# Optimization experiments

Measured on AMD Instinct MI355X. Metric: run time of the kernel, lower is better.

## Reference

```python
import jax, jax.numpy as jnp
from jax import lax
import numpy as np

B, T, D, H, C = 256, 2048, 40, 128, 35
LN_EPS = 1e-5


def _uniform(key, shape, scale):
    return jax.random.uniform(key, shape, jnp.float32, -scale, scale)


def setup_inputs() -> dict:
    key = jax.random.key(0)
    ks = jax.random.split(key, 16)
    s = 1.0 / np.sqrt(H)  # PyTorch LSTM init scale
    inp = {
        "x": jax.random.normal(ks[0], (B, T, D), jnp.float32),
        "length": jax.random.randint(ks[1], (B,), 1, T + 1, jnp.int32),
        # layer 0 (input_size=D)
        "W_ih0": _uniform(ks[2], (4 * H, D), s),
        "W_hh0": _uniform(ks[3], (4 * H, H), s),
        "b_ih0": _uniform(ks[4], (4 * H,), s),
        "b_hh0": _uniform(ks[5], (4 * H,), s),
        # layer 1 (input_size=H)
        "W_ih1": _uniform(ks[6], (4 * H, H), s),
        "W_hh1": _uniform(ks[7], (4 * H, H), s),
        "b_ih1": _uniform(ks[8], (4 * H,), s),
        "b_hh1": _uniform(ks[9], (4 * H,), s),
        # LayerNorm + Linear head
        "ln_gamma": jnp.ones((H,), jnp.float32),
        "ln_beta": jnp.zeros((H,), jnp.float32),
        "fc_w": _uniform(ks[10], (C, H), 1.0 / np.sqrt(H)),
        "fc_b": _uniform(ks[11], (C,), 1.0 / np.sqrt(H)),
    }
    return inp


def _lstm_layer(xs, length, W_ih, W_hh, b_ih, b_hh):
    # xs: [T, B, D_in]; masked recurrence emulates pack_padded_sequence:
    # state is frozen for t >= length, so the final h equals the state at
    # each sequence's last valid step.
    Tn, Bn = xs.shape[0], xs.shape[1]
    Hn = W_hh.shape[1]
    h0 = jnp.zeros((Bn, Hn), xs.dtype)
    c0 = jnp.zeros((Bn, Hn), xs.dtype)

    def step(carry, inp):
        h, c = carry
        x_t, t = inp
        gates = x_t @ W_ih.T + b_ih + h @ W_hh.T + b_hh  # [B, 4H]
        i, f, g, o = jnp.split(gates, 4, axis=-1)  # PyTorch gate order i,f,g,o
        i = jax.nn.sigmoid(i)
        f = jax.nn.sigmoid(f)
        g = jnp.tanh(g)
        o = jax.nn.sigmoid(o)
        c_new = f * c + i * g
        h_new = o * jnp.tanh(c_new)
        m = (t < length)[:, None]
        h = jnp.where(m, h_new, h)
        c = jnp.where(m, c_new, c)
        return (h, c), h

    (h_fin, c_fin), hs = lax.scan(step, (h0, c0), (xs, jnp.arange(Tn)))
    return hs, h_fin


def reference(x, length, W_ih0, W_hh0, b_ih0, b_hh0, W_ih1, W_hh1, b_ih1, b_hh1,
              ln_gamma, ln_beta, fc_w, fc_b):
    xs = jnp.transpose(x, (1, 0, 2))  # [T, B, D]
    hs1, _ = _lstm_layer(xs, length, W_ih0, W_hh0, b_ih0, b_hh0)
    _, h_last = _lstm_layer(hs1, length, W_ih1, W_hh1, b_ih1, b_hh1)  # h[-1]: [B, H]
    # LayerNorm over feature dim
    mu = jnp.mean(h_last, axis=-1, keepdims=True)
    var = jnp.mean(jnp.square(h_last - mu), axis=-1, keepdims=True)
    hn = (h_last - mu) * lax.rsqrt(var + LN_EPS) * ln_gamma + ln_beta
    return hn @ fc_w.T + fc_b  # [B, C]
```

## Files before the change

### kernel.cpp

```cpp
#include <hip/hip_runtime.h>

#define Bn 256
#define Tn 2048
#define Dn 40
#define Hn 128
#define Cn 35

typedef _Float16 h2 __attribute__((ext_vector_type(2)));

__device__ __forceinline__ int sdot4(int a, int b, int c) {
#if __has_builtin(__builtin_amdgcn_sdot4)
  return __builtin_amdgcn_sdot4(a, b, c, false);
#else
  int r = c;
#pragma unroll
  for (int i = 0; i < 4; ++i)
    r += ((int)(a << (24 - 8 * i)) >> 24) * ((int)(b << (24 - 8 * i)) >> 24);
  return r;
#endif
}

__device__ __forceinline__ float fdot2f(h2 a, h2 b, float c) {
#if __has_builtin(__builtin_amdgcn_fdot2)
  return __builtin_amdgcn_fdot2(a, b, c, false);
#else
  return c + (float)(a[0]) * (float)(b[0]) + (float)(a[1]) * (float)(b[1]);
#endif
}

__device__ __forceinline__ h2 bch(int u) { return __builtin_bit_cast(h2, u); }

__device__ __forceinline__ int pk2i(float a, float b) {
  h2 r; r[0] = (_Float16)a; r[1] = (_Float16)b;
  return __builtin_bit_cast(int, r);
}

__device__ __forceinline__ float rcpf_(float x) {
#if __has_builtin(__builtin_amdgcn_rcpf)
  return __builtin_amdgcn_rcpf(x);
#else
  return 1.f / x;
#endif
}

__device__ __forceinline__ float sigm(float v) {
  v = fmaxf(fminf(v, 60.f), -60.f);
  return rcpf_(1.f + __expf(-v));
}

__device__ __forceinline__ float tanha(float v) {
  v = fmaxf(fminf(v, 15.f), -15.f);
  const float e = __expf(2.f * v);
  return (e - 1.f) * rcpf_(e + 1.f);
}

__device__ __forceinline__ int q8c(float v) {
  v = fminf(fmaxf(v, -127.f), 127.f);
  return (int)__builtin_rintf(v);
}

__device__ __forceinline__ int pk4(int a, int b, int c, int d) {
  return (a & 255) | ((b & 255) << 8) | ((c & 255) << 16) | (d << 24);
}

#if __has_builtin(__builtin_amdgcn_global_load_lds)
#define HAVE_GLDS 1
__device__ __forceinline__ void gl_lds16(const float* g, float* l) {
  __builtin_amdgcn_global_load_lds(
      (const __attribute__((address_space(1))) unsigned int*)(const void*)g,
      (__attribute__((address_space(3))) unsigned int*)(void*)l, 16, 0, 0);
}
#endif

__device__ __forceinline__ void quantW128(const float* __restrict__ p,
                                          int* __restrict__ q, float& sc) {
  float m = 1e-30f;
#pragma unroll
  for (int i = 0; i < 32; ++i) {
    const float4 v = reinterpret_cast<const float4*>(p)[i];
    m = fmaxf(m, fmaxf(fmaxf(fabsf(v.x), fabsf(v.y)),
                       fmaxf(fabsf(v.z), fabsf(v.w))));
  }
  const float inv = 127.f / m;
  sc = m * (1.f / 127.f);
#pragma unroll
  for (int i = 0; i < 32; ++i) {
    const float4 v = reinterpret_cast<const float4*>(p)[i];
    q[i] = pk4(q8c(v.x * inv), q8c(v.y * inv), q8c(v.z * inv), q8c(v.w * inv));
  }
}

#define RLST(w) __builtin_amdgcn_readlane(                                  \
    ((w) < 64 ? st0 : (w) < 128 ? st1 : (w) < 192 ? st2 : (w) < 256 ? st3  \
                                                        : st4), (w) & 63)

__global__ __launch_bounds__(512) void lstm2_fused(
    const float* __restrict__ x,
    const int*   __restrict__ length,
    const float* __restrict__ Wih0, const float* __restrict__ Whh0,
    const float* __restrict__ bih0, const float* __restrict__ bhh0,
    const float* __restrict__ Wih1, const float* __restrict__ Whh1,
    const float* __restrict__ bih1, const float* __restrict__ bhh1,
    const float* __restrict__ gam,  const float* __restrict__ bet,
    const float* __restrict__ fcw,  const float* __restrict__ fcb,
    float* __restrict__ out)
{
  __shared__ int   s_w0x[20][512];
  __shared__ __align__(16) float s_xraw[192 * 4];
  __shared__ int   s_xh2[2][320];
  __shared__ float s_xp[2][16][512];
  __shared__ float s_p0[4][132];
  __shared__ float s_p1[4][132];
  __shared__ int   s_hq[64];
  __shared__ float s_h1f[128];
  __shared__ float s_hn[128];

  const int tid  = threadIdx.x;
  const int lane = tid & 63;
  const int b    = blockIdx.x;
  const int len  = length[b];

  if (tid >= 256 && tid < 448) {
    const int seg0 = (tid >> 6) - 4;
    int seg = seg0 * 64 + lane;
    if (seg >= 160) seg = 0;
#if HAVE_GLDS
    gl_lds16(x + (size_t)b * Tn * Dn + seg * 4, &s_xraw[seg0 * 256]);
#else
    *(float4*)&s_xraw[seg * 4] =
        *(const float4*)(x + (size_t)b * Tn * Dn + seg * 4);
#endif
  }

  int q0h[32], q1x[32], q1h[32];
  float s0h, s1x, s1h;
  quantW128(Whh0 + (size_t)tid * Hn, q0h, s0h);
  quantW128(Wih1 + (size_t)tid * Hn, q1x, s1x);
  quantW128(Whh1 + (size_t)tid * Hn, q1h, s1h);
  s0h *= (1.f / 127.f);
  s1x *= (1.f / 127.f);
  s1h *= (1.f / 127.f);
  {
    const float* p = Wih0 + (size_t)tid * Dn;
#pragma unroll
    for (int k = 0; k < 20; ++k) s_w0x[k][tid] = pk2i(p[2 * k], p[2 * k + 1]);
  }
  const float bias0 = bih0[tid] + bhh0[tid];
  const float bias1 = bih1[tid] + bhh1[tid];

  float c0 = 0.f;
  float c1 = 0.f;

  if (tid < 64) s_hq[tid] = 0;
  __syncthreads();

  auto burst = [&](int bb) {
    const int* flat = &s_xh2[bb][0];
    const int st0 = flat[lane], st1 = flat[lane + 64], st2 = flat[lane + 128],
              st3 = flat[lane + 192], st4 = flat[lane + 256];
#pragma unroll
    for (int pass = 0; pass < 4; ++pass) {
      float a0 = 0.f, a1 = 0.f, a2 = 0.f, a3 = 0.f;
      const int r0 = pass * 4;
#pragma unroll
      for (int g = 0; g < 5; ++g) {
        const h2 w0 = bch(s_w0x[4 * g + 0][tid]);
        const h2 w1 = bch(s_w0x[4 * g + 1][tid]);
        const h2 w2 = bch(s_w0x[4 * g + 2][tid]);
        const h2 w3 = bch(s_w0x[4 * g + 3][tid]);
        a0 = fdot2f(bch(RLST(20 * (r0 + 0) + 4 * g + 0)), w0, a0);
        a0 = fdot2f(bch(RLST(20 * (r0 + 0) + 4 * g + 1)), w1, a0);
        a0 = fdot2f(bch(RLST(20 * (r0 + 0) + 4 * g + 2)), w2, a0);
        a0 = fdot2f(bch(RLST(20 * (r0 + 0) + 4 * g + 3)), w3, a0);
        a1 = fdot2f(bch(RLST(20 * (r0 + 1) + 4 * g + 0)), w0, a1);
        a1 = fdot2f(bch(RLST(20 * (r0 + 1) + 4 * g + 1)), w1, a1);
        a1 = fdot2f(bch(RLST(20 * (r0 + 1) + 4 * g + 2)), w2, a1);
        a1 = fdot2f(bch(RLST(20 * (r0 + 1) + 4 * g + 3)), w3, a1);
        a2 = fdot2f(bch(RLST(20 * (r0 + 2) + 4 * g + 0)), w0, a2);
        a2 = fdot2f(bch(RLST(20 * (r0 + 2) + 4 * g + 1)), w1, a2);
        a2 = fdot2f(bch(RLST(20 * (r0 + 2) + 4 * g + 2)), w2, a2);
        a2 = fdot2f(bch(RLST(20 * (r0 + 2) + 4 * g + 3)), w3, a2);
        a3 = fdot2f(bch(RLST(20 * (r0 + 3) + 4 * g + 0)), w0, a3);
        a3 = fdot2f(bch(RLST(20 * (r0 + 3) + 4 * g + 1)), w1, a3);
        a3 = fdot2f(bch(RLST(20 * (r0 + 3) + 4 * g + 2)), w2, a3);
        a3 = fdot2f(bch(RLST(20 * (r0 + 3) + 4 * g + 3)), w3, a3);
      }
      s_xp[bb][r0 + 0][tid] = a0;
      s_xp[bb][r0 + 1][tid] = a1;
      s_xp[bb][r0 + 2][tid] = a2;
      s_xp[bb][r0 + 3][tid] = a3;
    }
  };

  if (tid >= 256 && tid < 416) {
    const int u = tid - 256;
    const float4 v = *(const float4*)&s_xraw[4 * u];
    s_xh2[0][2 * u]     = pk2i(v.x, v.y);
    s_xh2[0][2 * u + 1] = pk2i(v.z, v.w);
  }
  __syncthreads();
  burst(0);
  __syncthreads();
  s_p0[tid >> 7][tid & 127] = bias0 + s_xp[0][0][tid];
  __syncthreads();

#pragma unroll 1
  for (int t = 0; t < len; ++t) {
    const int tl = t & 15;

    if (tid < 128) {
      const float gi = s_p0[0][tid], gf = s_p0[1][tid];
      const float gg = s_p0[2][tid], go = s_p0[3][tid];
      c0 = sigm(gf) * c0 + sigm(gi) * tanha(gg);
      const float h = sigm(go) * tanha(c0);
      ((signed char*)s_hq)[tid] = (signed char)(int)__builtin_rintf(h * 127.f);
    } else if (tid < 256) {
      if (t > 0) {
        const int u = tid - 128;
        const float gi = s_p1[0][u], gf = s_p1[1][u];
        const float gg = s_p1[2][u], go = s_p1[3][u];
        c1 = sigm(gf) * c1 + sigm(gi) * tanha(gg);
        const float h = sigm(go) * tanha(c1);
        ((signed char*)s_hq)[128 + u] =
            (signed char)(int)__builtin_rintf(h * 127.f);
      }
    } else if (tid < 416 && tl == 13) {
      const int u = tid - 256;
      const float4 v = *(const float4*)&s_xraw[4 * u];
      const int nb = ((t + 3) >> 4) & 1;
      s_xh2[nb][2 * u]     = pk2i(v.x, v.y);
      s_xh2[nb][2 * u + 1] = pk2i(v.z, v.w);
    }
    __syncthreads();

    const int vq = s_hq[lane];

    if (tid >= 256 && tid < 448 && tl == 12) {
      const int t0 = (t & ~15) + 16;
      if (t0 <= Tn - 16) {
        const int seg0 = (tid >> 6) - 4;
        int seg = seg0 * 64 + lane;
        if (seg >= 160) seg = 0;
#if HAVE_GLDS
        gl_lds16(x + ((size_t)b * Tn + t0) * Dn + seg * 4,
                 &s_xraw[seg0 * 256]);
#else
        *(float4*)&s_xraw[seg * 4] =
            *(const float4*)(x + ((size_t)b * Tn + t0) * Dn + seg * 4);
#endif
      }
    }

    const int rowi = t + 1;
    const float xacc = s_xp[(rowi >> 4) & 1][rowi & 15][tid];

    int ia = 0, ia2 = 0, ib = 0, ib2 = 0, ic = 0, ic2 = 0;
#pragma unroll
    for (int j = 0; j < 32; j += 2) {
      const int s0 = __builtin_amdgcn_readlane(vq, j);
      const int s1 = __builtin_amdgcn_readlane(vq, j + 1);
      ia  = sdot4(s0, q0h[j], ia);
      ib  = sdot4(s0, q1x[j], ib);
      ia2 = sdot4(s1, q0h[j + 1], ia2);
      ib2 = sdot4(s1, q1x[j + 1], ib2);
    }
#pragma unroll
    for (int j = 0; j < 32; j += 2) {
      const int s0 = __builtin_amdgcn_readlane(vq, 32 + j);
      const int s1 = __builtin_amdgcn_readlane(vq, 33 + j);
      ic  = sdot4(s0, q1h[j], ic);
      ic2 = sdot4(s1, q1h[j + 1], ic2);
    }
    s_p0[tid >> 7][tid & 127] = bias0 + xacc + (float)(ia + ia2) * s0h;
    s_p1[tid >> 7][tid & 127] =
        bias1 + (float)(ib + ib2) * s1x + (float)(ic + ic2) * s1h;

    if (tl == 14) burst(((t + 2) >> 4) & 1);
    __syncthreads();
  }

  if (tid >= 128 && tid < 256) {
    const int u = tid - 128;
    const float gi = s_p1[0][u], gf = s_p1[1][u];
    const float gg = s_p1[2][u], go = s_p1[3][u];
    c1 = sigm(gf) * c1 + sigm(gi) * tanha(gg);
    s_h1f[u] = sigm(go) * tanha(c1);
  }
  __syncthreads();

  if (tid < 64) {
    const float a = s_h1f[tid], d = s_h1f[64 + tid];
    float s = a + d, q = a * a + d * d;
#pragma unroll
    for (int m = 32; m >= 1; m >>= 1) {
      s += __shfl_xor(s, m, 64);
      q += __shfl_xor(q, m, 64);
    }
    const float mu = s * (1.f / 128.f);
    float var = q * (1.f / 128.f) - mu * mu;
    var = fmaxf(var, 0.f);
    const float rstd = rsqrtf(var + 1e-5f);
    s_hn[tid]      = (a - mu) * rstd * gam[tid]      + bet[tid];
    s_hn[64 + tid] = (d - mu) * rstd * gam[64 + tid] + bet[64 + tid];
  }
  __syncthreads();

  if (tid < Cn) {
    float acc = fcb[tid];
    const float* wp = fcw + tid * Hn;
#pragma unroll 4
    for (int k = 0; k < Hn; ++k) acc += s_hn[k] * wp[k];
    out[(size_t)b * Cn + tid] = acc;
  }
}

extern "C" void kernel_launch(void* const* d_in, const int* in_sizes, int n_in,
                              void* d_out, int out_size, void* d_ws, size_t ws_size,
                              hipStream_t stream) {
  (void)in_sizes; (void)n_in; (void)d_ws; (void)ws_size; (void)out_size;
  lstm2_fused<<<dim3(Bn), dim3(512), 0, stream>>>(
      (const float*)d_in[0],  (const int*)d_in[1],
      (const float*)d_in[2],  (const float*)d_in[3],
      (const float*)d_in[4],  (const float*)d_in[5],
      (const float*)d_in[6],  (const float*)d_in[7],
      (const float*)d_in[8],  (const float*)d_in[9],
      (const float*)d_in[10], (const float*)d_in[11],
      (const float*)d_in[12], (const float*)d_in[13],
      (float*)d_out);
}
```

Baseline: 2.512 ms.

## Split LSTM layers across waves with shuffle gate exchange and one barrier per step

Reassigns the work so waves 0-3 own layer 0 and waves 4-7 own layer 1. Each lane computes two gate rows and exchanges gates with its partner lane through a cross-lane shuffle, instead of writing gate pre-activations to shared memory and re-reading them after a barrier. The hidden-state buffer is double-buffered, which cuts the barriers per timestep from two to one; the raw barrier is issued with an explicit waitcnt. The cost is imbalance: layer-1 waves now do twice the dot-product work of layer-0 waves, and register pressure rises with four quantized weight arrays per lane.

```diff
diff --git a/kernel.cpp b/kernel.cpp
--- a/kernel.cpp
+++ b/kernel.cpp
@@ -109,19 +109,23 @@
   __shared__ __align__(16) float s_xraw[192 * 4];
   __shared__ int   s_xh2[2][320];
   __shared__ float s_xp[2][16][512];
-  __shared__ float s_p0[4][132];
-  __shared__ float s_p1[4][132];
-  __shared__ int   s_hq[64];
+  __shared__ int   s_hq[2][64];
   __shared__ float s_h1f[128];
   __shared__ float s_hn[128];
 
   const int tid  = threadIdx.x;
   const int lane = tid & 63;
+  const int wv   = tid >> 6;
   const int b    = blockIdx.x;
   const int len  = length[b];
 
-  if (tid >= 256 && tid < 448) {
-    const int seg0 = (tid >> 6) - 4;
+  const bool isL1 = (wv >= 4);
+  const int  u    = ((wv & 3) << 5) | (lane & 31);
+  const int  rA   = ((lane < 32) ? 0 : 256) + u;
+  const int  rB   = rA + 128;
+
+  if (tid < 192) {
+    const int seg0 = wv;
     int seg = seg0 * 64 + lane;
     if (seg >= 160) seg = 0;
 #if HAVE_GLDS
@@ -132,26 +136,33 @@
 #endif
   }
 
-  int q0h[32], q1x[32], q1h[32];
-  float s0h, s1x, s1h;
-  quantW128(Whh0 + (size_t)tid * Hn, q0h, s0h);
-  quantW128(Wih1 + (size_t)tid * Hn, q1x, s1x);
-  quantW128(Whh1 + (size_t)tid * Hn, q1h, s1h);
-  s0h *= (1.f / 127.f);
-  s1x *= (1.f / 127.f);
-  s1h *= (1.f / 127.f);
+  int qA[32], qB[32], qC[32], qD[32];
+  float scA, scB, scC = 0.f, scD = 0.f;
+  float biasA, biasB;
+  if (!isL1) {
+    quantW128(Whh0 + (size_t)rA * Hn, qA, scA);
+    quantW128(Whh0 + (size_t)rB * Hn, qB, scB);
+    biasA = bih0[rA] + bhh0[rA];
+    biasB = bih0[rB] + bhh0[rB];
+  } else {
+    quantW128(Wih1 + (size_t)rA * Hn, qA, scA);
+    quantW128(Wih1 + (size_t)rB * Hn, qB, scB);
+    quantW128(Whh1 + (size_t)rA * Hn, qC, scC);
+    quantW128(Whh1 + (size_t)rB * Hn, qD, scD);
+    biasA = bih1[rA] + bhh1[rA];
+    biasB = bih1[rB] + bhh1[rB];
+  }
+  scA *= (1.f / 127.f);
+  scB *= (1.f / 127.f);
+  scC *= (1.f / 127.f);
+  scD *= (1.f / 127.f);
   {
     const float* p = Wih0 + (size_t)tid * Dn;
 #pragma unroll
     for (int k = 0; k < 20; ++k) s_w0x[k][tid] = pk2i(p[2 * k], p[2 * k + 1]);
   }
-  const float bias0 = bih0[tid] + bhh0[tid];
-  const float bias1 = bih1[tid] + bhh1[tid];
-
-  float c0 = 0.f;
-  float c1 = 0.f;
-
-  if (tid < 64) s_hq[tid] = 0;
+  if (tid < 128) s_hq[tid >> 6][tid & 63] = 0;
+  float creg = 0.f;
   __syncthreads();
 
   auto burst = [&](int bb) {
@@ -192,53 +203,24 @@
     }
   };
 
-  if (tid >= 256 && tid < 416) {
-    const int u = tid - 256;
-    const float4 v = *(const float4*)&s_xraw[4 * u];
-    s_xh2[0][2 * u]     = pk2i(v.x, v.y);
-    s_xh2[0][2 * u + 1] = pk2i(v.z, v.w);
+  if (tid < 160) {
+    const float4 v = *(const float4*)&s_xraw[4 * tid];
+    s_xh2[0][2 * tid]     = pk2i(v.x, v.y);
+    s_xh2[0][2 * tid + 1] = pk2i(v.z, v.w);
   }
   __syncthreads();
   burst(0);
-  __syncthreads();
-  s_p0[tid >> 7][tid & 127] = bias0 + s_xp[0][0][tid];
   __syncthreads();
 
 #pragma unroll 1
   for (int t = 0; t < len; ++t) {
     const int tl = t & 15;
-
-    if (tid < 128) {
-      const float gi = s_p0[0][tid], gf = s_p0[1][tid];
-      const float gg = s_p0[2][tid], go = s_p0[3][tid];
-      c0 = sigm(gf) * c0 + sigm(gi) * tanha(gg);
-      const float h = sigm(go) * tanha(c0);
-      ((signed char*)s_hq)[tid] = (signed char)(int)__builtin_rintf(h * 127.f);
-    } else if (tid < 256) {
-      if (t > 0) {
-        const int u = tid - 128;
-        const float gi = s_p1[0][u], gf = s_p1[1][u];
-        const float gg = s_p1[2][u], go = s_p1[3][u];
-        c1 = sigm(gf) * c1 + sigm(gi) * tanha(gg);
-        const float h = sigm(go) * tanha(c1);
-        ((signed char*)s_hq)[128 + u] =
-            (signed char)(int)__builtin_rintf(h * 127.f);
-      }
-    } else if (tid < 416 && tl == 13) {
-      const int u = tid - 256;
-      const float4 v = *(const float4*)&s_xraw[4 * u];
-      const int nb = ((t + 3) >> 4) & 1;
-      s_xh2[nb][2 * u]     = pk2i(v.x, v.y);
-      s_xh2[nb][2 * u + 1] = pk2i(v.z, v.w);
-    }
-    __syncthreads();
-
-    const int vq = s_hq[lane];
-
-    if (tid >= 256 && tid < 448 && tl == 12) {
+    const int vq = s_hq[t & 1][lane];
+
+    if (tl == 12 && tid < 192) {
       const int t0 = (t & ~15) + 16;
       if (t0 <= Tn - 16) {
-        const int seg0 = (tid >> 6) - 4;
+        const int seg0 = wv;
         int seg = seg0 * 64 + lane;
         if (seg >= 160) seg = 0;
 #if HAVE_GLDS
@@ -250,41 +232,112 @@
 #endif
       }
     }
-
-    const int rowi = t + 1;
-    const float xacc = s_xp[(rowi >> 4) & 1][rowi & 15][tid];
-
-    int ia = 0, ia2 = 0, ib = 0, ib2 = 0, ic = 0, ic2 = 0;
+    if (tl == 13 && tid < 160) {
+#if HAVE_GLDS
+      asm volatile("s_waitcnt vmcnt(0)" ::: "memory");
+#endif
+      const float4 v = *(const float4*)&s_xraw[4 * tid];
+      const int nb = ((t + 3) >> 4) & 1;
+      s_xh2[nb][2 * tid]     = pk2i(v.x, v.y);
+      s_xh2[nb][2 * tid + 1] = pk2i(v.z, v.w);
+    }
+
+    float gv1, gv2;
+    if (!isL1) {
+      int ia = 0, ia2 = 0, ib = 0, ib2 = 0;
+#pragma unroll
+      for (int j = 0; j < 32; j += 2) {
+        const int s0 = __builtin_amdgcn_readlane(vq, j);
+        const int s1 = __builtin_amdgcn_readlane(vq, j + 1);
+        ia  = sdot4(s0, qA[j],     ia);
+        ib  = sdot4(s0, qB[j],     ib);
+        ia2 = sdot4(s1, qA[j + 1], ia2);
+        ib2 = sdot4(s1, qB[j + 1], ib2);
+      }
+      const float xa = s_xp[(t >> 4) & 1][tl][rA];
+      const float xb = s_xp[(t >> 4) & 1][tl][rB];
+      gv1 = biasA + xa + (float)(ia + ia2) * scA;
+      gv2 = biasB + xb + (float)(ib + ib2) * scB;
+    } else {
+      int ia = 0, ia2 = 0, ib = 0, ib2 = 0, ic = 0, ic2 = 0, id_ = 0, id2 = 0;
+#pragma unroll
+      for (int j = 0; j < 32; j += 2) {
+        const int s0 = __builtin_amdgcn_readlane(vq, j);
+        const int s1 = __builtin_amdgcn_readlane(vq, j + 1);
+        ia  = sdot4(s0, qA[j],     ia);
+        ib  = sdot4(s0, qB[j],     ib);
+        ia2 = sdot4(s1, qA[j + 1], ia2);
+        ib2 = sdot4(s1, qB[j + 1], ib2);
+      }
+#pragma unroll
+      for (int j = 0; j < 32; j += 2) {
+        const int s0 = __builtin_amdgcn_readlane(vq, 32 + j);
+        const int s1 = __builtin_amdgcn_readlane(vq, 33 + j);
+        ic  = sdot4(s0, qC[j],     ic);
+        id_ = sdot4(s0, qD[j],     id_);
+        ic2 = sdot4(s1, qC[j + 1], ic2);
+        id2 = sdot4(s1, qD[j + 1], id2);
+      }
+      gv1 = biasA + (float)(ia + ia2) * scA + (float)(ic + ic2) * scC;
+      gv2 = biasB + (float)(ib + ib2) * scB + (float)(id_ + id2) * scD;
+    }
+
+    const float p1 = __shfl_xor(gv1, 32, 64);
+    const float p2 = __shfl_xor(gv2, 32, 64);
+    const bool  lo = (lane < 32);
+    const float gi = lo ? gv1 : p1;
+    const float gf = lo ? gv2 : p2;
+    const float gg = lo ? p1 : gv1;
+    const float go = lo ? p2 : gv2;
+
+    if (!isL1 || t > 0) {
+      creg = sigm(gf) * creg + sigm(gi) * tanha(gg);
+      const float h = sigm(go) * tanha(creg);
+      if (lo)
+        ((signed char*)s_hq)[(((t + 1) & 1) << 8) + (isL1 ? 128 : 0) + u] =
+            (signed char)(int)__builtin_rintf(h * 127.f);
+    }
+
+    if (tl == 14) burst(((t + 2) >> 4) & 1);
+
+    asm volatile("s_waitcnt lgkmcnt(0)" ::: "memory");
+    __builtin_amdgcn_s_barrier();
+    __builtin_amdgcn_sched_barrier(0);
+  }
+
+  if (isL1) {
+    const int vq = s_hq[len & 1][lane];
+    int ia = 0, ia2 = 0, ib = 0, ib2 = 0, ic = 0, ic2 = 0, id_ = 0, id2 = 0;
 #pragma unroll
     for (int j = 0; j < 32; j += 2) {
       const int s0 = __builtin_amdgcn_readlane(vq, j);
       const int s1 = __builtin_amdgcn_readlane(vq, j + 1);
-      ia  = sdot4(s0, q0h[j], ia);
-      ib  = sdot4(s0, q1x[j], ib);
-      ia2 = sdot4(s1, q0h[j + 1], ia2);
-      ib2 = sdot4(s1, q1x[j + 1], ib2);
+      ia  = sdot4(s0, qA[j],     ia);
+      ib  = sdot4(s0, qB[j],     ib);
+      ia2 = sdot4(s1, qA[j + 1], ia2);
+      ib2 = sdot4(s1, qB[j + 1], ib2);
     }
 #pragma unroll
     for (int j = 0; j < 32; j += 2) {
       const int s0 = __builtin_amdgcn_readlane(vq, 32 + j);
       const int s1 = __builtin_amdgcn_readlane(vq, 33 + j);
-      ic  = sdot4(s0, q1h[j], ic);
-      ic2 = sdot4(s1, q1h[j + 1], ic2);
-    }
-    s_p0[tid >> 7][tid & 127] = bias0 + xacc + (float)(ia + ia2) * s0h;
-    s_p1[tid >> 7][tid & 127] =
-        bias1 + (float)(ib + ib2) * s1x + (float)(ic + ic2) * s1h;
-
-    if (tl == 14) burst(((t + 2) >> 4) & 1);
-    __syncthreads();
-  }
-
-  if (tid >= 128 && tid < 256) {
-    const int u = tid - 128;
-    const float gi = s_p1[0][u], gf = s_p1[1][u];
-    const float gg = s_p1[2][u], go = s_p1[3][u];
-    c1 = sigm(gf) * c1 + sigm(gi) * tanha(gg);
-    s_h1f[u] = sigm(go) * tanha(c1);
+      ic  = sdot4(s0, qC[j],     ic);
+      id_ = sdot4(s0, qD[j],     id_);
+      ic2 = sdot4(s1, qC[j + 1], ic2);
+      id2 = sdot4(s1, qD[j + 1], id2);
+    }
+    float gv1 = biasA + (float)(ia + ia2) * scA + (float)(ic + ic2) * scC;
+    float gv2 = biasB + (float)(ib + ib2) * scB + (float)(id_ + id2) * scD;
+    const float p1 = __shfl_xor(gv1, 32, 64);
+    const float p2 = __shfl_xor(gv2, 32, 64);
+    const bool  lo = (lane < 32);
+    const float gi = lo ? gv1 : p1;
+    const float gf = lo ? gv2 : p2;
+    const float gg = lo ? p1 : gv1;
+    const float go = lo ? p2 : gv2;
+    creg = sigm(gf) * creg + sigm(gi) * tanha(gg);
+    const float h = sigm(go) * tanha(creg);
+    if (lo) s_h1f[u] = h;
   }
   __syncthreads();
 
```

New measurement: 2.614 ms. 4.1% more time.

## Replace block barriers with per-wave flag-based pipeline across LSTM layers

Applied to the files above, without the earlier changes.

Each wave now has a fixed role. Waves 0-1 run the layer-0 recurrence over all four gates, waves 2-3 run the layer-1 recurrence, and waves 4-7 compute the layer-1 input projection from h0 and the x-projection bursts. The per-step __syncthreads is replaced by LDS progress flags that each wave polls with spin-waits, so layer 1 can trail layer 0 by up to four steps through a ring buffer of terms. This removes full-block barriers and the extra shared-memory round trip for gates, at the cost of busy-wait polling, more registers per thread, and subtle ordering risks in the hand-written LDS flag protocol.

```diff
diff --git a/kernel.cpp b/kernel.cpp
--- a/kernel.cpp
+++ b/kernel.cpp
@@ -7,6 +7,9 @@
 #define Cn 35
 
 typedef _Float16 h2 __attribute__((ext_vector_type(2)));
+typedef int int4v __attribute__((ext_vector_type(4)));
+
+__device__ __forceinline__ int imin(int a, int b) { return a < b ? a : b; }
 
 __device__ __forceinline__ int sdot4(int a, int b, int c) {
 #if __has_builtin(__builtin_amdgcn_sdot4)
@@ -105,23 +108,24 @@
     const float* __restrict__ fcw,  const float* __restrict__ fcb,
     float* __restrict__ out)
 {
-  __shared__ int   s_w0x[20][512];
   __shared__ __align__(16) float s_xraw[192 * 4];
   __shared__ int   s_xh2[2][320];
   __shared__ float s_xp[2][16][512];
-  __shared__ float s_p0[4][132];
-  __shared__ float s_p1[4][132];
-  __shared__ int   s_hq[64];
+  __shared__ float s_term[4][128][4];
+  __shared__ int   s_h0q[2][32];
+  __shared__ int   s_h1q[2][32];
+  __shared__ __align__(32) int s_flag[8];
   __shared__ float s_h1f[128];
   __shared__ float s_hn[128];
 
   const int tid  = threadIdx.x;
   const int lane = tid & 63;
+  const int wv   = tid >> 6;
   const int b    = blockIdx.x;
   const int len  = length[b];
 
-  if (tid >= 256 && tid < 448) {
-    const int seg0 = (tid >> 6) - 4;
+  if (wv >= 4 && wv <= 6) {
+    const int seg0 = wv - 4;
     int seg = seg0 * 64 + lane;
     if (seg >= 160) seg = 0;
 #if HAVE_GLDS
@@ -131,161 +135,260 @@
         *(const float4*)(x + (size_t)b * Tn * Dn + seg * 4);
 #endif
   }
-
-  int q0h[32], q1x[32], q1h[32];
-  float s0h, s1x, s1h;
-  quantW128(Whh0 + (size_t)tid * Hn, q0h, s0h);
-  quantW128(Wih1 + (size_t)tid * Hn, q1x, s1x);
-  quantW128(Whh1 + (size_t)tid * Hn, q1h, s1h);
-  s0h *= (1.f / 127.f);
-  s1x *= (1.f / 127.f);
-  s1h *= (1.f / 127.f);
-  {
-    const float* p = Wih0 + (size_t)tid * Dn;
-#pragma unroll
-    for (int k = 0; k < 20; ++k) s_w0x[k][tid] = pk2i(p[2 * k], p[2 * k + 1]);
-  }
-  const float bias0 = bih0[tid] + bhh0[tid];
-  const float bias1 = bih1[tid] + bhh1[tid];
-
-  float c0 = 0.f;
-  float c1 = 0.f;
-
-  if (tid < 64) s_hq[tid] = 0;
+  if (tid < 32) {
+    s_h0q[0][tid] = 0; s_h0q[1][tid] = 0;
+    s_h1q[0][tid] = 0; s_h1q[1][tid] = 0;
+  }
+  if (tid < 8) s_flag[tid] = 0;
+
+  int qq0[32], qq1[32], qq2[32], qq3[32];
+  int wpa[20], wpb[20];
+  float sc0 = 0.f, sc1 = 0.f, sc2 = 0.f, sc3 = 0.f;
+  float bs0 = 0.f, bs1 = 0.f, bs2 = 0.f, bs3 = 0.f;
+
+  if (wv < 2) {
+    const int u = (wv << 6) | lane;
+    quantW128(Whh0 + (size_t)(u)       * Hn, qq0, sc0);
+    quantW128(Whh0 + (size_t)(u + 128) * Hn, qq1, sc1);
+    quantW128(Whh0 + (size_t)(u + 256) * Hn, qq2, sc2);
+    quantW128(Whh0 + (size_t)(u + 384) * Hn, qq3, sc3);
+    bs0 = bih0[u]       + bhh0[u];
+    bs1 = bih0[u + 128] + bhh0[u + 128];
+    bs2 = bih0[u + 256] + bhh0[u + 256];
+    bs3 = bih0[u + 384] + bhh0[u + 384];
+  } else if (wv < 4) {
+    const int u = ((wv - 2) << 6) | lane;
+    quantW128(Whh1 + (size_t)(u)       * Hn, qq0, sc0);
+    quantW128(Whh1 + (size_t)(u + 128) * Hn, qq1, sc1);
+    quantW128(Whh1 + (size_t)(u + 256) * Hn, qq2, sc2);
+    quantW128(Whh1 + (size_t)(u + 384) * Hn, qq3, sc3);
+  } else {
+    const int hl = ((wv - 4) << 6) | lane;
+    quantW128(Wih1 + (size_t)hl * Hn, qq0, sc0);
+    quantW128(Wih1 + (size_t)(hl + 256) * Hn, qq1, sc1);
+    bs0 = bih1[hl]       + bhh1[hl];
+    bs1 = bih1[hl + 256] + bhh1[hl + 256];
+    const float* p0 = Wih0 + (size_t)hl * Dn;
+    const float* p1 = Wih0 + (size_t)(hl + 256) * Dn;
+#pragma unroll
+    for (int k = 0; k < 20; ++k) {
+      wpa[k] = pk2i(p0[2 * k], p0[2 * k + 1]);
+      wpb[k] = pk2i(p1[2 * k], p1[2 * k + 1]);
+    }
+  }
+  sc0 *= (1.f / 127.f);
+  sc1 *= (1.f / 127.f);
+  sc2 *= (1.f / 127.f);
+  sc3 *= (1.f / 127.f);
+
   __syncthreads();
 
-  auto burst = [&](int bb) {
-    const int* flat = &s_xh2[bb][0];
+  if (wv >= 4) {
+    const int hl = ((wv - 4) << 6) | lane;
+    if (hl < 160) {
+      const float4 v = *(const float4*)&s_xraw[4 * hl];
+      s_xh2[0][2 * hl]     = pk2i(v.x, v.y);
+      s_xh2[0][2 * hl + 1] = pk2i(v.z, v.w);
+    }
+  }
+  __syncthreads();
+
+  if (wv >= 4) {
+    const int hl = ((wv - 4) << 6) | lane;
+    const int* flat = &s_xh2[0][0];
     const int st0 = flat[lane], st1 = flat[lane + 64], st2 = flat[lane + 128],
               st3 = flat[lane + 192], st4 = flat[lane + 256];
-#pragma unroll
-    for (int pass = 0; pass < 4; ++pass) {
-      float a0 = 0.f, a1 = 0.f, a2 = 0.f, a3 = 0.f;
-      const int r0 = pass * 4;
-#pragma unroll
-      for (int g = 0; g < 5; ++g) {
-        const h2 w0 = bch(s_w0x[4 * g + 0][tid]);
-        const h2 w1 = bch(s_w0x[4 * g + 1][tid]);
-        const h2 w2 = bch(s_w0x[4 * g + 2][tid]);
-        const h2 w3 = bch(s_w0x[4 * g + 3][tid]);
-        a0 = fdot2f(bch(RLST(20 * (r0 + 0) + 4 * g + 0)), w0, a0);
-        a0 = fdot2f(bch(RLST(20 * (r0 + 0) + 4 * g + 1)), w1, a0);
-        a0 = fdot2f(bch(RLST(20 * (r0 + 0) + 4 * g + 2)), w2, a0);
-        a0 = fdot2f(bch(RLST(20 * (r0 + 0) + 4 * g + 3)), w3, a0);
-        a1 = fdot2f(bch(RLST(20 * (r0 + 1) + 4 * g + 0)), w0, a1);
-        a1 = fdot2f(bch(RLST(20 * (r0 + 1) + 4 * g + 1)), w1, a1);
-        a1 = fdot2f(bch(RLST(20 * (r0 + 1) + 4 * g + 2)), w2, a1);
-        a1 = fdot2f(bch(RLST(20 * (r0 + 1) + 4 * g + 3)), w3, a1);
-        a2 = fdot2f(bch(RLST(20 * (r0 + 2) + 4 * g + 0)), w0, a2);
-        a2 = fdot2f(bch(RLST(20 * (r0 + 2) + 4 * g + 1)), w1, a2);
-        a2 = fdot2f(bch(RLST(20 * (r0 + 2) + 4 * g + 2)), w2, a2);
-        a2 = fdot2f(bch(RLST(20 * (r0 + 2) + 4 * g + 3)), w3, a2);
-        a3 = fdot2f(bch(RLST(20 * (r0 + 3) + 4 * g + 0)), w0, a3);
-        a3 = fdot2f(bch(RLST(20 * (r0 + 3) + 4 * g + 1)), w1, a3);
-        a3 = fdot2f(bch(RLST(20 * (r0 + 3) + 4 * g + 2)), w2, a3);
-        a3 = fdot2f(bch(RLST(20 * (r0 + 3) + 4 * g + 3)), w3, a3);
-      }
-      s_xp[bb][r0 + 0][tid] = a0;
-      s_xp[bb][r0 + 1][tid] = a1;
-      s_xp[bb][r0 + 2][tid] = a2;
-      s_xp[bb][r0 + 3][tid] = a3;
-    }
-  };
-
-  if (tid >= 256 && tid < 416) {
-    const int u = tid - 256;
-    const float4 v = *(const float4*)&s_xraw[4 * u];
-    s_xh2[0][2 * u]     = pk2i(v.x, v.y);
-    s_xh2[0][2 * u + 1] = pk2i(v.z, v.w);
+#pragma unroll 1
+    for (int r = 0; r < 16; ++r) {
+      float a0 = 0.f, a1 = 0.f;
+#pragma unroll
+      for (int w = 0; w < 20; ++w) {
+        const h2 s = bch(RLST(20 * r + w));
+        a0 = fdot2f(s, bch(wpa[w]), a0);
+        a1 = fdot2f(s, bch(wpb[w]), a1);
+      }
+      s_xp[0][r][hl]       = a0;
+      s_xp[0][r][hl + 256] = a1;
+    }
   }
   __syncthreads();
-  burst(0);
-  __syncthreads();
-  s_p0[tid >> 7][tid & 127] = bias0 + s_xp[0][0][tid];
-  __syncthreads();
-
+
+  const __attribute__((address_space(3))) int* flagp3 =
+      (const __attribute__((address_space(3))) int*)(const void*)s_flag;
+  int4v f03 = {0, 0, 0, 0}, f47 = {0, 0, 0, 0};
+
+#define READFLAGS()                                                          \
+  asm volatile("ds_read_b128 %0, %2\n\tds_read_b128 %1, %2 offset:16\n\t"    \
+               "s_waitcnt lgkmcnt(0)"                                        \
+               : "=v"(f03), "=v"(f47) : "v"(flagp3) : "memory")
+#define HMIN4 imin(imin(f47[0], f47[1]), imin(f47[2], f47[3]))
+#define PUBLISH(val)                                                         \
+  do {                                                                       \
+    asm volatile("s_waitcnt lgkmcnt(0)" ::: "memory");                       \
+    ((volatile int*)s_flag)[wv] = (val);                                     \
+  } while (0)
+
+  if (wv < 2) {
+    const int u = (wv << 6) | lane;
+    float c0 = 0.f;
 #pragma unroll 1
-  for (int t = 0; t < len; ++t) {
-    const int tl = t & 15;
-
-    if (tid < 128) {
-      const float gi = s_p0[0][tid], gf = s_p0[1][tid];
-      const float gg = s_p0[2][tid], go = s_p0[3][tid];
+    for (int t = 0; t < len; ++t) {
+      const int tl = t & 15;
+      const int needH = t - (tl == 0 ? 0 : 1);
+      {
+        int pf = (wv == 0) ? f03[1] : f03[0];
+        if (!(pf >= t && HMIN4 >= needH)) {
+          for (;;) {
+            READFLAGS();
+            pf = (wv == 0) ? f03[1] : f03[0];
+            if (pf >= t && HMIN4 >= needH) break;
+            __builtin_amdgcn_s_sleep(1);
+          }
+        }
+      }
+      const int vq = s_h0q[(t + 1) & 1][lane & 31];
+      const int cs = (t >> 4) & 1;
+      const float xI = s_xp[cs][tl][u];
+      const float xF = s_xp[cs][tl][u + 128];
+      const float xG = s_xp[cs][tl][u + 256];
+      const float xO = s_xp[cs][tl][u + 384];
+      int aI = 0, aF = 0, aG = 0, aO = 0;
+#pragma unroll
+      for (int j = 0; j < 32; ++j) {
+        const int s = __builtin_amdgcn_readlane(vq, j);
+        aI = sdot4(s, qq0[j], aI);
+        aF = sdot4(s, qq1[j], aF);
+        aG = sdot4(s, qq2[j], aG);
+        aO = sdot4(s, qq3[j], aO);
+      }
+      const float gi = bs0 + xI + (float)aI * sc0;
+      const float gf = bs1 + xF + (float)aF * sc1;
+      const float gg = bs2 + xG + (float)aG * sc2;
+      const float go = bs3 + xO + (float)aO * sc3;
       c0 = sigm(gf) * c0 + sigm(gi) * tanha(gg);
       const float h = sigm(go) * tanha(c0);
-      ((signed char*)s_hq)[tid] = (signed char)(int)__builtin_rintf(h * 127.f);
-    } else if (tid < 256) {
-      if (t > 0) {
-        const int u = tid - 128;
-        const float gi = s_p1[0][u], gf = s_p1[1][u];
-        const float gg = s_p1[2][u], go = s_p1[3][u];
-        c1 = sigm(gf) * c1 + sigm(gi) * tanha(gg);
-        const float h = sigm(go) * tanha(c1);
-        ((signed char*)s_hq)[128 + u] =
-            (signed char)(int)__builtin_rintf(h * 127.f);
-      }
-    } else if (tid < 416 && tl == 13) {
-      const int u = tid - 256;
-      const float4 v = *(const float4*)&s_xraw[4 * u];
-      const int nb = ((t + 3) >> 4) & 1;
-      s_xh2[nb][2 * u]     = pk2i(v.x, v.y);
-      s_xh2[nb][2 * u + 1] = pk2i(v.z, v.w);
-    }
-    __syncthreads();
-
-    const int vq = s_hq[lane];
-
-    if (tid >= 256 && tid < 448 && tl == 12) {
-      const int t0 = (t & ~15) + 16;
-      if (t0 <= Tn - 16) {
-        const int seg0 = (tid >> 6) - 4;
-        int seg = seg0 * 64 + lane;
-        if (seg >= 160) seg = 0;
+      ((signed char*)s_h0q)[((t & 1) << 7) + u] =
+          (signed char)(int)__builtin_rintf(h * 127.f);
+      PUBLISH(t + 1);
+      READFLAGS();
+    }
+  } else if (wv < 4) {
+    const int u = ((wv - 2) << 6) | lane;
+    float c1 = 0.f;
+#pragma unroll 1
+    for (int t = 0; t < len; ++t) {
+      {
+        int pf = (wv == 2) ? f03[3] : f03[2];
+        if (!(pf >= t && HMIN4 >= t + 1)) {
+          for (;;) {
+            READFLAGS();
+            pf = (wv == 2) ? f03[3] : f03[2];
+            if (pf >= t && HMIN4 >= t + 1) break;
+            __builtin_amdgcn_s_sleep(1);
+          }
+        }
+      }
+      const int vq = s_h1q[(t + 1) & 1][lane & 31];
+      const float4 tv = *(const float4*)&s_term[t & 3][u][0];
+      int aI = 0, aF = 0, aG = 0, aO = 0;
+#pragma unroll
+      for (int j = 0; j < 32; ++j) {
+        const int s = __builtin_amdgcn_readlane(vq, j);
+        aI = sdot4(s, qq0[j], aI);
+        aF = sdot4(s, qq1[j], aF);
+        aG = sdot4(s, qq2[j], aG);
+        aO = sdot4(s, qq3[j], aO);
+      }
+      const float gi = tv.x + (float)aI * sc0;
+      const float gf = tv.y + (float)aF * sc1;
+      const float gg = tv.z + (float)aG * sc2;
+      const float go = tv.w + (float)aO * sc3;
+      c1 = sigm(gf) * c1 + sigm(gi) * tanha(gg);
+      const float h = sigm(go) * tanha(c1);
+      if (t == len - 1) s_h1f[u] = h;
+      ((signed char*)s_h1q)[((t & 1) << 7) + u] =
+          (signed char)(int)__builtin_rintf(h * 127.f);
+      PUBLISH(t + 1);
+      READFLAGS();
+    }
+  } else {
+    const int hl   = ((wv - 4) << 6) | lane;
+    const int u    = hl & 127;
+    const int gsel = hl >> 7;
+#pragma unroll 1
+    for (int t = 0; t < len; ++t) {
+      const int tl = t & 15;
+      const int needX = (tl == 5) ? (t - 5) : (tl == 8) ? t : -1000000000;
+      if (!(f03[0] >= t + 1 && f03[1] >= t + 1 &&
+            f03[2] >= t - 3 && f03[3] >= t - 3 && HMIN4 >= needX)) {
+        for (;;) {
+          READFLAGS();
+          if (f03[0] >= t + 1 && f03[1] >= t + 1 &&
+              f03[2] >= t - 3 && f03[3] >= t - 3 && HMIN4 >= needX) break;
+          __builtin_amdgcn_s_sleep(1);
+        }
+      }
+      if (tl == 2 && wv <= 6) {
+        const int t0 = (t & ~15) + 16;
+        if (t0 <= Tn - 16) {
+          const int seg0 = wv - 4;
+          int seg = seg0 * 64 + lane;
+          if (seg >= 160) seg = 0;
 #if HAVE_GLDS
-        gl_lds16(x + ((size_t)b * Tn + t0) * Dn + seg * 4,
-                 &s_xraw[seg0 * 256]);
+          gl_lds16(x + ((size_t)b * Tn + t0) * Dn + seg * 4,
+                   &s_xraw[seg0 * 256]);
 #else
-        *(float4*)&s_xraw[seg * 4] =
-            *(const float4*)(x + ((size_t)b * Tn + t0) * Dn + seg * 4);
-#endif
-      }
-    }
-
-    const int rowi = t + 1;
-    const float xacc = s_xp[(rowi >> 4) & 1][rowi & 15][tid];
-
-    int ia = 0, ia2 = 0, ib = 0, ib2 = 0, ic = 0, ic2 = 0;
-#pragma unroll
-    for (int j = 0; j < 32; j += 2) {
-      const int s0 = __builtin_amdgcn_readlane(vq, j);
-      const int s1 = __builtin_amdgcn_readlane(vq, j + 1);
-      ia  = sdot4(s0, q0h[j], ia);
-      ib  = sdot4(s0, q1x[j], ib);
-      ia2 = sdot4(s1, q0h[j + 1], ia2);
-      ib2 = sdot4(s1, q1x[j + 1], ib2);
-    }
-#pragma unroll
-    for (int j = 0; j < 32; j += 2) {
-      const int s0 = __builtin_amdgcn_readlane(vq, 32 + j);
-      const int s1 = __builtin_amdgcn_readlane(vq, 33 + j);
-      ic  = sdot4(s0, q1h[j], ic);
-      ic2 = sdot4(s1, q1h[j + 1], ic2);
-    }
-    s_p0[tid >> 7][tid & 127] = bias0 + xacc + (float)(ia + ia2) * s0h;
-    s_p1[tid >> 7][tid & 127] =
-        bias1 + (float)(ib + ib2) * s1x + (float)(ic + ic2) * s1h;
-
-    if (tl == 14) burst(((t + 2) >> 4) & 1);
-    __syncthreads();
-  }
-
-  if (tid >= 128 && tid < 256) {
-    const int u = tid - 128;
-    const float gi = s_p1[0][u], gf = s_p1[1][u];
-    const float gg = s_p1[2][u], go = s_p1[3][u];
-    c1 = sigm(gf) * c1 + sigm(gi) * tanha(gg);
-    s_h1f[u] = sigm(go) * tanha(c1);
-  }
+          *(float4*)&s_xraw[seg * 4] =
+              *(const float4*)(x + ((size_t)b * Tn + t0) * Dn + seg * 4);
+#endif
+        }
+      }
+      const int vq = s_h0q[t & 1][lane & 31];
+      int aA = 0, aB = 0;
+#pragma unroll
+      for (int j = 0; j < 32; ++j) {
+        const int s = __builtin_amdgcn_readlane(vq, j);
+        aA = sdot4(s, qq0[j], aA);
+        aB = sdot4(s, qq1[j], aB);
+      }
+      s_term[t & 3][u][gsel]     = bs0 + (float)aA * sc0;
+      s_term[t & 3][u][gsel + 2] = bs1 + (float)aB * sc1;
+      if (tl == 5 && wv <= 6) {
+#if HAVE_GLDS
+        asm volatile("s_waitcnt vmcnt(0)" ::: "memory");
+#endif
+        if (hl < 160) {
+          const float4 v = *(const float4*)&s_xraw[4 * hl];
+          const int nb = ((t >> 4) & 1) ^ 1;
+          s_xh2[nb][2 * hl]     = pk2i(v.x, v.y);
+          s_xh2[nb][2 * hl + 1] = pk2i(v.z, v.w);
+        }
+      }
+      if (tl >= 8) {
+        const int nb = ((t >> 4) & 1) ^ 1;
+        const int r0 = (tl - 8) * 2;
+        const int* flat = &s_xh2[nb][0];
+        const int st0 = flat[lane], st1 = flat[lane + 64],
+                  st2 = flat[lane + 128], st3 = flat[lane + 192],
+                  st4 = flat[lane + 256];
+#pragma unroll
+        for (int r = r0; r < r0 + 2; ++r) {
+          float a0 = 0.f, a1 = 0.f;
+#pragma unroll
+          for (int w = 0; w < 20; ++w) {
+            const h2 s = bch(RLST(20 * r + w));
+            a0 = fdot2f(s, bch(wpa[w]), a0);
+            a1 = fdot2f(s, bch(wpb[w]), a1);
+          }
+          s_xp[nb][r][hl]       = a0;
+          s_xp[nb][r][hl + 256] = a1;
+        }
+      }
+      PUBLISH(t + 1);
+      READFLAGS();
+    }
+  }
+
   __syncthreads();
 
   if (tid < 64) {
```

Result: slower. 3.892 ms (+54.9%).
